# Optimization experiments

Measured on AMD Instinct MI355X. Metric: run time of the kernel, lower is better.

Reference implementation:

```python
import jax, jax.numpy as jnp
import numpy as np

N_NODES = 50000
N_EDGES = 800000
D_IN = 128
H = 4
F = 16


def setup_inputs() -> dict:
    key = jax.random.key(0)
    k1, k2, k3, k4 = jax.random.split(key, 4)
    feat = jax.random.normal(k1, (N_NODES, D_IN), dtype=jnp.float32)
    W = jax.random.normal(k2, (D_IN, H * F), dtype=jnp.float32) / np.sqrt(D_IN)
    src = jax.random.randint(k3, (N_EDGES,), 0, N_NODES, dtype=jnp.int32)
    dst = jax.random.randint(k4, (N_EDGES,), 0, N_NODES, dtype=jnp.int32)
    return {"feat": feat, "W": W, "src": src, "dst": dst}


def reference(feat, W, src, dst):
    # Project: [N, D_in] @ [D_in, H*F] -> [N, H, F]
    ft = (feat @ W).reshape(N_NODES, H, F)
    # Per-edge dot-product scores, scaled: [E, H]
    e = jnp.einsum('ehf,ehf->eh', ft[src], ft[dst]) / np.sqrt(F).astype(np.float32)
    # Segment (per-destination) softmax over incoming edges
    seg_max = jax.ops.segment_max(e, dst, num_segments=N_NODES)  # [N, H]
    ex = jnp.exp(e - seg_max[dst])
    denom = jax.ops.segment_sum(ex, dst, num_segments=N_NODES)  # [N, H]
    sa = ex / denom[dst]  # [E, H]
    # Weighted scatter-sum of source features: [N, H, F]
    msgs = ft[src] * sa[:, :, None]
    out = jax.ops.segment_sum(msgs, dst, num_segments=N_NODES)
    return out
```

## Files before the change

### kernel.cpp

```cpp
#include <hip/hip_runtime.h>
#include <hip/hip_fp16.h>

#define N_NODES 50000
#define N_EDGES 800000
#define D_IN 128
#define HH 4
#define FF 16
#define HF 64
#define NBUCKETS 196
#define BCAP 4608
#define CHUNK 2048
#define NBIN_BLOCKS ((N_EDGES + CHUNK - 1) / CHUNK)
#define GEMM_BLOCKS ((N_NODES + 63) / 64)
#define SORT_K ((BCAP + 255) / 256)

struct __align__(8) Half4 { __half2 a, b; };

typedef _Float16 half2_v __attribute__((ext_vector_type(2)));
struct __align__(8) H4 { half2_v a, b; };

__device__ __forceinline__ float dot4h(H4 a, H4 v) {
#if __has_builtin(__builtin_amdgcn_fdot2)
    return __builtin_amdgcn_fdot2(a.a, v.a,
           __builtin_amdgcn_fdot2(a.b, v.b, 0.0f, false), false);
#else
    return (float)a.a[0] * (float)v.a[0] + (float)a.a[1] * (float)v.a[1]
         + (float)a.b[0] * (float)v.b[0] + (float)a.b[1] * (float)v.b[1];
#endif
}

__device__ __forceinline__ int block_excl_scan(int val, int* wsum) {
    int lane = threadIdx.x & 63;
    int wave = threadIdx.x >> 6;
    int incl = val;
#pragma unroll
    for (int off = 1; off < 64; off <<= 1) {
        int t = __shfl_up(incl, off, 64);
        if (lane >= off) incl += t;
    }
    if (lane == 63) wsum[wave] = incl;
    __syncthreads();
    if (threadIdx.x == 0) {
        int a = 0;
#pragma unroll
        for (int w = 0; w < 4; ++w) { int t = wsum[w]; wsum[w] = a; a += t; }
    }
    __syncthreads();
    return incl + wsum[wave] - val;
}

__global__ __launch_bounds__(256, 2) void gemm_kernel(const float* __restrict__ feat,
                                                      const float* __restrict__ W,
                                                      __half* __restrict__ fth) {
    __shared__ float As[64][132];
    __shared__ float Bs[D_IN][HF];

    {
        const float4* W4 = (const float4*)W;
        float4* B4 = (float4*)Bs;
#pragma unroll
        for (int i = 0; i < 8; ++i) {
            int idx = threadIdx.x + 256 * i;
            B4[idx] = W4[idx];
        }
    }
    {
        int row0 = blockIdx.x * 64;
        const float4* F4 = (const float4*)feat;
#pragma unroll
        for (int i = 0; i < 8; ++i) {
            int idx = threadIdx.x + 256 * i;
            int r = idx >> 5;
            int c4 = idx & 31;
            float4 v = make_float4(0.f, 0.f, 0.f, 0.f);
            int row = row0 + r;
            if (row < N_NODES) v = F4[(size_t)row * 32 + c4];
            *(float4*)&As[r][c4 * 4] = v;
        }
    }
    __syncthreads();

    const int tr = threadIdx.x >> 4;
    const int tc = threadIdx.x & 15;

    float acc[4][4] = {};
#pragma unroll 8
    for (int k = 0; k < D_IN; k += 4) {
        float av[4][4], bv[4][4];
#pragma unroll
        for (int i = 0; i < 4; ++i) {
            float4 a = *(const float4*)&As[tr * 4 + i][k];
            av[i][0] = a.x; av[i][1] = a.y; av[i][2] = a.z; av[i][3] = a.w;
        }
#pragma unroll
        for (int j = 0; j < 4; ++j) {
            float4 b = *(const float4*)&Bs[k + j][tc * 4];
            bv[j][0] = b.x; bv[j][1] = b.y; bv[j][2] = b.z; bv[j][3] = b.w;
        }
#pragma unroll
        for (int i = 0; i < 4; ++i)
#pragma unroll
            for (int j = 0; j < 4; ++j)
#pragma unroll
                for (int c = 0; c < 4; ++c)
                    acc[i][c] = fmaf(av[i][j], bv[j][c], acc[i][c]);
    }

    int row0 = blockIdx.x * 64;
#pragma unroll
    for (int i = 0; i < 4; ++i) {
        int row = row0 + tr * 4 + i;
        if (row < N_NODES) {
            Half4 h;
            h.a = __floats2half2_rn(acc[i][0], acc[i][1]);
            h.b = __floats2half2_rn(acc[i][2], acc[i][3]);
            *(Half4*)&fth[(size_t)row * HF + tc * 4] = h;
        }
    }
}

__global__ __launch_bounds__(256) void bin_kernel(const int* __restrict__ src,
                                                  const int* __restrict__ dst,
                                                  int* __restrict__ gcur,
                                                  int* __restrict__ recs) {
    __shared__ int hist[256];
    __shared__ int offs[256];
    __shared__ int cur[256];
    __shared__ int gbase[256];
    __shared__ int wsum[4];
    __shared__ int lrec[CHUNK];

    int tid = threadIdx.x;
    int e0 = blockIdx.x * CHUNK;
    int n = N_EDGES - e0; if (n > CHUNK) n = CHUNK;

    hist[tid] = 0;
    __syncthreads();

    int myrec[CHUNK / 256];
    int myb[CHUNK / 256];
#pragma unroll
    for (int k = 0; k < CHUNK / 256; ++k) {
        int idx = tid + k * 256;
        myb[k] = -1;
        if (idx < n) {
            int s = src[e0 + idx];
            int d = dst[e0 + idx];
            int b = d >> 8;
            myrec[k] = s | ((d & 255) << 16) | (b << 24);
            myb[k] = b;
            atomicAdd(&hist[b], 1);
        }
    }
    __syncthreads();

    int val = hist[tid];
    int excl = block_excl_scan(val, wsum);
    offs[tid] = excl;
    cur[tid] = excl;
    if (val > 0) gbase[tid] = atomicAdd(&gcur[tid], val);
    __syncthreads();

#pragma unroll
    for (int k = 0; k < CHUNK / 256; ++k) {
        if (myb[k] >= 0) {
            int p = atomicAdd(&cur[myb[k]], 1);
            lrec[p] = myrec[k];
        }
    }
    __syncthreads();

    for (int i = tid; i < n; i += 256) {
        int r = lrec[i];
        int b = (r >> 24) & 255;
        int pos = gbase[b] + (i - offs[b]);
        if (pos < BCAP) recs[(size_t)b * BCAP + pos] = r;
    }
}

__global__ __launch_bounds__(256) void sort_kernel(const int* __restrict__ gcur,
                                                   const int* __restrict__ recs,
                                                   int* __restrict__ csr,
                                                   int* __restrict__ row_beg,
                                                   int* __restrict__ row_end) {
    __shared__ int lhist[256];
    __shared__ int lcur[256];
    __shared__ int wsum[4];

    int tid = threadIdx.x;
    int b = blockIdx.x;
    int cnt = gcur[b]; if (cnt > BCAP) cnt = BCAP;
    const int* rp = recs + (size_t)b * BCAP;

    lhist[tid] = 0;
    __syncthreads();

    int rk[SORT_K];
#pragma unroll
    for (int k = 0; k < SORT_K; ++k) {
        int i = tid + k * 256;
        bool valid = i < cnt;
        rk[k] = valid ? rp[i] : 0;
        if (valid) atomicAdd(&lhist[(rk[k] >> 16) & 255], 1);
    }
    __syncthreads();

    int val = lhist[tid];
    int excl = block_excl_scan(val, wsum);
    lcur[tid] = excl;
    __syncthreads();

    int base = b * BCAP;
#pragma unroll
    for (int k = 0; k < SORT_K; ++k) {
        int i = tid + k * 256;
        if (i < cnt) {
            int p = atomicAdd(&lcur[(rk[k] >> 16) & 255], 1);
            csr[base + p] = rk[k] & 0xFFFF;
        }
    }

    int node = (b << 8) + tid;
    if (node < N_NODES) {
        row_beg[node] = base + excl;
        row_end[node] = base + excl + val;
    }
}

__global__ __launch_bounds__(256) void gather_kernel(const __half* __restrict__ fth,
                                                     const int* __restrict__ row_beg,
                                                     const int* __restrict__ row_end,
                                                     const int* __restrict__ csr,
                                                     float* __restrict__ out) {
    int node = __builtin_amdgcn_readfirstlane(blockIdx.x * 4 + (threadIdx.x >> 6));
    int lane = threadIdx.x & 63;
    int g = lane >> 4;
    int hl = lane & 15;

    int beg = row_beg[node];
    int end = row_end[node];

    H4 a = *(const H4*)&fth[(size_t)node * HF + 4 * hl];

    float acc0 = 0.f, acc1 = 0.f, acc2 = 0.f, acc3 = 0.f, lsum = 0.f;

    for (int i = beg; i < end; i += 8) {
        int idx0 = i + g;
        int idx1 = i + 4 + g;
        bool act0 = idx0 < end;
        bool act1 = idx1 < end;
        int s0 = csr[act0 ? idx0 : beg];
        int s1 = csr[act1 ? idx1 : beg];
        H4 v0 = *(const H4*)&fth[(size_t)s0 * HF + 4 * hl];
        H4 v1 = *(const H4*)&fth[(size_t)s1 * HF + 4 * hl];

        float p0 = dot4h(a, v0);
        float p1 = dot4h(a, v1);
        p0 += __shfl_xor(p0, 1, 64);  p1 += __shfl_xor(p1, 1, 64);
        p0 += __shfl_xor(p0, 2, 64);  p1 += __shfl_xor(p1, 2, 64);

        float w0 = act0 ? __expf(p0 * 0.25f) : 0.0f;
        float w1 = act1 ? __expf(p1 * 0.25f) : 0.0f;

        acc0 = fmaf(w0, (float)v0.a[0], acc0);
        acc1 = fmaf(w0, (float)v0.a[1], acc1);
        acc2 = fmaf(w0, (float)v0.b[0], acc2);
        acc3 = fmaf(w0, (float)v0.b[1], acc3);
        acc0 = fmaf(w1, (float)v1.a[0], acc0);
        acc1 = fmaf(w1, (float)v1.a[1], acc1);
        acc2 = fmaf(w1, (float)v1.b[0], acc2);
        acc3 = fmaf(w1, (float)v1.b[1], acc3);
        lsum += w0 + w1;
    }

    acc0 += __shfl_xor(acc0, 16, 64);  acc0 += __shfl_xor(acc0, 32, 64);
    acc1 += __shfl_xor(acc1, 16, 64);  acc1 += __shfl_xor(acc1, 32, 64);
    acc2 += __shfl_xor(acc2, 16, 64);  acc2 += __shfl_xor(acc2, 32, 64);
    acc3 += __shfl_xor(acc3, 16, 64);  acc3 += __shfl_xor(acc3, 32, 64);
    lsum += __shfl_xor(lsum, 16, 64);  lsum += __shfl_xor(lsum, 32, 64);

    if (lane < 16) {
        float inv = (lsum > 0.0f) ? 1.0f / lsum : 0.0f;
        *(float4*)&out[(size_t)node * HF + 4 * hl] =
            make_float4(acc0 * inv, acc1 * inv, acc2 * inv, acc3 * inv);
    }
}

extern "C" void kernel_launch(void* const* d_in, const int* in_sizes, int n_in,
                              void* d_out, int out_size, void* d_ws, size_t ws_size,
                              hipStream_t stream) {
    const float* feat = (const float*)d_in[0];
    const float* W = (const float*)d_in[1];
    const int* src = (const int*)d_in[2];
    const int* dst = (const int*)d_in[3];
    float* out = (float*)d_out;

    __half* fth = (__half*)d_ws;
    int* recs = (int*)(fth + (size_t)N_NODES * HF);
    int* csr = recs + (size_t)NBUCKETS * BCAP;
    int* row_beg = csr + (size_t)NBUCKETS * BCAP;
    int* row_end = row_beg + N_NODES;
    int* gcur = row_end + N_NODES;

    hipMemsetAsync(gcur, 0, NBUCKETS * sizeof(int), stream);
    gemm_kernel<<<GEMM_BLOCKS, 256, 0, stream>>>(feat, W, fth);
    bin_kernel<<<NBIN_BLOCKS, 256, 0, stream>>>(src, dst, gcur, recs);
    sort_kernel<<<NBUCKETS, 256, 0, stream>>>(gcur, recs, csr, row_beg, row_end);
    gather_kernel<<<N_NODES * 64 / 256, 256, 0, stream>>>(fth, row_beg, row_end, csr, out);
}
```

Measured before the change: 142.9 us.

## Fuse GEMM and edge binning into one launch; compact CSR and row ranges

```diff
diff --git a/kernel.cpp b/kernel.cpp
--- a/kernel.cpp
+++ b/kernel.cpp
@@ -49,140 +49,145 @@
     return incl + wsum[wave] - val;
 }
 
-__global__ __launch_bounds__(256, 2) void gemm_kernel(const float* __restrict__ feat,
-                                                      const float* __restrict__ W,
-                                                      __half* __restrict__ fth) {
-    __shared__ float As[64][132];
-    __shared__ float Bs[D_IN][HF];
-
-    {
-        const float4* W4 = (const float4*)W;
-        float4* B4 = (float4*)Bs;
-#pragma unroll
-        for (int i = 0; i < 8; ++i) {
-            int idx = threadIdx.x + 256 * i;
-            B4[idx] = W4[idx];
-        }
-    }
-    {
-        int row0 = blockIdx.x * 64;
-        const float4* F4 = (const float4*)feat;
-#pragma unroll
-        for (int i = 0; i < 8; ++i) {
-            int idx = threadIdx.x + 256 * i;
-            int r = idx >> 5;
-            int c4 = idx & 31;
-            float4 v = make_float4(0.f, 0.f, 0.f, 0.f);
-            int row = row0 + r;
-            if (row < N_NODES) v = F4[(size_t)row * 32 + c4];
-            *(float4*)&As[r][c4 * 4] = v;
-        }
-    }
-    __syncthreads();
-
-    const int tr = threadIdx.x >> 4;
-    const int tc = threadIdx.x & 15;
-
-    float acc[4][4] = {};
+union SmemU {
+    struct {
+        float As[64][132];
+        float Bs[D_IN][HF];
+    } g;
+    struct {
+        int hist[256], offs[256], cur[256], gbase[256];
+        int wsum[4];
+        int lrec[CHUNK];
+    } b;
+};
+
+__global__ __launch_bounds__(256, 2) void gemm_bin_kernel(const float* __restrict__ feat,
+                                                          const float* __restrict__ W,
+                                                          const int* __restrict__ src,
+                                                          const int* __restrict__ dst,
+                                                          __half* __restrict__ fth,
+                                                          int* __restrict__ gcur,
+                                                          int* __restrict__ recs) {
+    __shared__ SmemU smem;
+    int tid = threadIdx.x;
+
+    if (blockIdx.x < NBIN_BLOCKS) {
+        int e0 = blockIdx.x * CHUNK;
+        int n = N_EDGES - e0; if (n > CHUNK) n = CHUNK;
+
+        smem.b.hist[tid] = 0;
+        __syncthreads();
+
+        int myrec[CHUNK / 256];
+        int myb[CHUNK / 256];
+#pragma unroll
+        for (int k = 0; k < CHUNK / 256; ++k) {
+            int idx = tid + k * 256;
+            myb[k] = -1;
+            if (idx < n) {
+                int s = src[e0 + idx];
+                int d = dst[e0 + idx];
+                int b = d >> 8;
+                myrec[k] = s | ((d & 255) << 16) | (b << 24);
+                myb[k] = b;
+                atomicAdd(&smem.b.hist[b], 1);
+            }
+        }
+        __syncthreads();
+
+        int val = smem.b.hist[tid];
+        int excl = block_excl_scan(val, smem.b.wsum);
+        smem.b.offs[tid] = excl;
+        smem.b.cur[tid] = excl;
+        if (val > 0) smem.b.gbase[tid] = atomicAdd(&gcur[tid], val);
+        __syncthreads();
+
+#pragma unroll
+        for (int k = 0; k < CHUNK / 256; ++k) {
+            if (myb[k] >= 0) {
+                int p = atomicAdd(&smem.b.cur[myb[k]], 1);
+                smem.b.lrec[p] = myrec[k];
+            }
+        }
+        __syncthreads();
+
+        for (int i = tid; i < n; i += 256) {
+            int r = smem.b.lrec[i];
+            int b = (r >> 24) & 255;
+            int pos = smem.b.gbase[b] + (i - smem.b.offs[b]);
+            if (pos < BCAP) recs[(size_t)b * BCAP + pos] = r;
+        }
+    } else {
+        int gb = blockIdx.x - NBIN_BLOCKS;
+        {
+            const float4* W4 = (const float4*)W;
+            float4* B4 = (float4*)smem.g.Bs;
+#pragma unroll
+            for (int i = 0; i < 8; ++i) {
+                int idx = tid + 256 * i;
+                B4[idx] = W4[idx];
+            }
+        }
+        {
+            int row0 = gb * 64;
+            const float4* F4 = (const float4*)feat;
+#pragma unroll
+            for (int i = 0; i < 8; ++i) {
+                int idx = tid + 256 * i;
+                int r = idx >> 5;
+                int c4 = idx & 31;
+                float4 v = make_float4(0.f, 0.f, 0.f, 0.f);
+                int row = row0 + r;
+                if (row < N_NODES) v = F4[(size_t)row * 32 + c4];
+                *(float4*)&smem.g.As[r][c4 * 4] = v;
+            }
+        }
+        __syncthreads();
+
+        const int tr = tid >> 4;
+        const int tc = tid & 15;
+
+        float acc[4][4] = {};
 #pragma unroll 8
-    for (int k = 0; k < D_IN; k += 4) {
-        float av[4][4], bv[4][4];
+        for (int k = 0; k < D_IN; k += 4) {
+            float av[4][4], bv[4][4];
+#pragma unroll
+            for (int i = 0; i < 4; ++i) {
+                float4 a = *(const float4*)&smem.g.As[tr * 4 + i][k];
+                av[i][0] = a.x; av[i][1] = a.y; av[i][2] = a.z; av[i][3] = a.w;
+            }
+#pragma unroll
+            for (int j = 0; j < 4; ++j) {
+                float4 b = *(const float4*)&smem.g.Bs[k + j][tc * 4];
+                bv[j][0] = b.x; bv[j][1] = b.y; bv[j][2] = b.z; bv[j][3] = b.w;
+            }
+#pragma unroll
+            for (int i = 0; i < 4; ++i)
+#pragma unroll
+                for (int j = 0; j < 4; ++j)
+#pragma unroll
+                    for (int c = 0; c < 4; ++c)
+                        acc[i][c] = fmaf(av[i][j], bv[j][c], acc[i][c]);
+        }
+
+        int row0 = gb * 64;
 #pragma unroll
         for (int i = 0; i < 4; ++i) {
-            float4 a = *(const float4*)&As[tr * 4 + i][k];
-            av[i][0] = a.x; av[i][1] = a.y; av[i][2] = a.z; av[i][3] = a.w;
-        }
-#pragma unroll
-        for (int j = 0; j < 4; ++j) {
-            float4 b = *(const float4*)&Bs[k + j][tc * 4];
-            bv[j][0] = b.x; bv[j][1] = b.y; bv[j][2] = b.z; bv[j][3] = b.w;
-        }
-#pragma unroll
-        for (int i = 0; i < 4; ++i)
-#pragma unroll
-            for (int j = 0; j < 4; ++j)
-#pragma unroll
-                for (int c = 0; c < 4; ++c)
-                    acc[i][c] = fmaf(av[i][j], bv[j][c], acc[i][c]);
-    }
-
-    int row0 = blockIdx.x * 64;
-#pragma unroll
-    for (int i = 0; i < 4; ++i) {
-        int row = row0 + tr * 4 + i;
-        if (row < N_NODES) {
-            Half4 h;
-            h.a = __floats2half2_rn(acc[i][0], acc[i][1]);
-            h.b = __floats2half2_rn(acc[i][2], acc[i][3]);
-            *(Half4*)&fth[(size_t)row * HF + tc * 4] = h;
-        }
-    }
-}
-
-__global__ __launch_bounds__(256) void bin_kernel(const int* __restrict__ src,
-                                                  const int* __restrict__ dst,
-                                                  int* __restrict__ gcur,
-                                                  int* __restrict__ recs) {
-    __shared__ int hist[256];
-    __shared__ int offs[256];
-    __shared__ int cur[256];
-    __shared__ int gbase[256];
-    __shared__ int wsum[4];
-    __shared__ int lrec[CHUNK];
-
-    int tid = threadIdx.x;
-    int e0 = blockIdx.x * CHUNK;
-    int n = N_EDGES - e0; if (n > CHUNK) n = CHUNK;
-
-    hist[tid] = 0;
-    __syncthreads();
-
-    int myrec[CHUNK / 256];
-    int myb[CHUNK / 256];
-#pragma unroll
-    for (int k = 0; k < CHUNK / 256; ++k) {
-        int idx = tid + k * 256;
-        myb[k] = -1;
-        if (idx < n) {
-            int s = src[e0 + idx];
-            int d = dst[e0 + idx];
-            int b = d >> 8;
-            myrec[k] = s | ((d & 255) << 16) | (b << 24);
-            myb[k] = b;
-            atomicAdd(&hist[b], 1);
-        }
-    }
-    __syncthreads();
-
-    int val = hist[tid];
-    int excl = block_excl_scan(val, wsum);
-    offs[tid] = excl;
-    cur[tid] = excl;
-    if (val > 0) gbase[tid] = atomicAdd(&gcur[tid], val);
-    __syncthreads();
-
-#pragma unroll
-    for (int k = 0; k < CHUNK / 256; ++k) {
-        if (myb[k] >= 0) {
-            int p = atomicAdd(&cur[myb[k]], 1);
-            lrec[p] = myrec[k];
-        }
-    }
-    __syncthreads();
-
-    for (int i = tid; i < n; i += 256) {
-        int r = lrec[i];
-        int b = (r >> 24) & 255;
-        int pos = gbase[b] + (i - offs[b]);
-        if (pos < BCAP) recs[(size_t)b * BCAP + pos] = r;
+            int row = row0 + tr * 4 + i;
+            if (row < N_NODES) {
+                Half4 h;
+                h.a = __floats2half2_rn(acc[i][0], acc[i][1]);
+                h.b = __floats2half2_rn(acc[i][2], acc[i][3]);
+                *(Half4*)&fth[(size_t)row * HF + tc * 4] = h;
+            }
+        }
     }
 }
 
 __global__ __launch_bounds__(256) void sort_kernel(const int* __restrict__ gcur,
                                                    const int* __restrict__ recs,
-                                                   int* __restrict__ csr,
-                                                   int* __restrict__ row_beg,
-                                                   int* __restrict__ row_end) {
+                                                   unsigned short* __restrict__ csr,
+                                                   int2* __restrict__ rows) {
     __shared__ int lhist[256];
     __shared__ int lcur[256];
     __shared__ int wsum[4];
@@ -216,29 +221,26 @@
         int i = tid + k * 256;
         if (i < cnt) {
             int p = atomicAdd(&lcur[(rk[k] >> 16) & 255], 1);
-            csr[base + p] = rk[k] & 0xFFFF;
+            csr[base + p] = (unsigned short)(rk[k] & 0xFFFF);
         }
     }
 
     int node = (b << 8) + tid;
-    if (node < N_NODES) {
-        row_beg[node] = base + excl;
-        row_end[node] = base + excl + val;
-    }
+    if (node < N_NODES) rows[node] = make_int2(base + excl, base + excl + val);
 }
 
 __global__ __launch_bounds__(256) void gather_kernel(const __half* __restrict__ fth,
-                                                     const int* __restrict__ row_beg,
-                                                     const int* __restrict__ row_end,
-                                                     const int* __restrict__ csr,
+                                                     const int2* __restrict__ rows,
+                                                     const unsigned short* __restrict__ csr,
                                                      float* __restrict__ out) {
     int node = __builtin_amdgcn_readfirstlane(blockIdx.x * 4 + (threadIdx.x >> 6));
     int lane = threadIdx.x & 63;
     int g = lane >> 4;
     int hl = lane & 15;
 
-    int beg = row_beg[node];
-    int end = row_end[node];
+    int2 be = rows[node];
+    int beg = be.x;
+    int end = be.y;
 
     H4 a = *(const H4*)&fth[(size_t)node * HF + 4 * hl];
 
@@ -297,14 +299,13 @@
 
     __half* fth = (__half*)d_ws;
     int* recs = (int*)(fth + (size_t)N_NODES * HF);
-    int* csr = recs + (size_t)NBUCKETS * BCAP;
-    int* row_beg = csr + (size_t)NBUCKETS * BCAP;
-    int* row_end = row_beg + N_NODES;
-    int* gcur = row_end + N_NODES;
+    unsigned short* csr = (unsigned short*)(recs + (size_t)NBUCKETS * BCAP);
+    int2* rows = (int2*)(csr + (size_t)NBUCKETS * BCAP);
+    int* gcur = (int*)(rows + N_NODES);
 
     hipMemsetAsync(gcur, 0, NBUCKETS * sizeof(int), stream);
-    gemm_kernel<<<GEMM_BLOCKS, 256, 0, stream>>>(feat, W, fth);
-    bin_kernel<<<NBIN_BLOCKS, 256, 0, stream>>>(src, dst, gcur, recs);
-    sort_kernel<<<NBUCKETS, 256, 0, stream>>>(gcur, recs, csr, row_beg, row_end);
-    gather_kernel<<<N_NODES * 64 / 256, 256, 0, stream>>>(fth, row_beg, row_end, csr, out);
-}
+    gemm_bin_kernel<<<NBIN_BLOCKS + GEMM_BLOCKS, 256, 0, stream>>>(feat, W, src, dst,
+                                                                   fth, gcur, recs);
+    sort_kernel<<<NBUCKETS, 256, 0, stream>>>(gcur, recs, csr, rows);
+    gather_kernel<<<N_NODES * 64 / 256, 256, 0, stream>>>(fth, rows, csr, out);
+}
```

New measurement: 142.5 us. No clear change (-0.3%).
